# Performance work log

Measured on AMD Instinct MI355X. Metric: run time of the kernel, lower is better.

## Reference

```python
import jax, jax.numpy as jnp
import numpy as np

IN_FEATURES = 4096
OUT_FEATURES = 4096
BANDWIDTH = min(IN_FEATURES, OUT_FEATURES) // 8  # 512, as in the torch default


def band_indices(n_out, n_in, bw):
    """Vectorized equivalent of BandMatrix.create_band_indices (COO row/col lists)."""
    i = np.arange(n_out)
    lo = np.maximum(0, i - bw)
    hi = np.minimum(n_in, i + bw + 1)
    counts = hi - lo
    total = int(counts.sum())
    rows = np.repeat(i, counts)
    start = np.cumsum(counts) - counts  # offset of each row's first entry
    cols = np.arange(total) - np.repeat(start, counts) + np.repeat(lo, counts)
    return rows.astype(np.int32), cols.astype(np.int32)


def setup_inputs() -> dict:
    key = jax.random.key(0)
    kx, kw = jax.random.split(key)
    rows_np, cols_np = band_indices(OUT_FEATURES, IN_FEATURES, BANDWIDTH)
    nnz = rows_np.shape[0]  # 3935744
    x = jax.random.normal(kx, (4, 2048, IN_FEATURES), dtype=jnp.float32)
    W_values = jax.random.normal(kw, (nnz,), dtype=jnp.float32)
    bias = jnp.zeros((OUT_FEATURES,), dtype=jnp.float32)
    return {
        "x": x,
        "W_values": W_values,
        "bias": bias,
        "rows": jnp.asarray(rows_np),
        "cols": jnp.asarray(cols_np),
    }


def reference(x, W_values, bias, rows, cols):
    # Densify banded COO weight [out, in] (matches sparse_coo_tensor().to_dense()).
    W = jnp.zeros((OUT_FEATURES, IN_FEATURES), dtype=W_values.dtype).at[rows, cols].set(W_values)
    # x: [B, S, in] @ W.T: [in, out] -> [B, S, out]
    out = jnp.einsum('bsi,oi->bso', x, W) + bias
    return out
```

## Files before the change

kernel.cpp:

```cpp
#include <hip/hip_runtime.h>
#include <stdint.h>

#define IN_F  4096
#define OUT_F 4096
#define BW    512
#define WB2   1280
#define BM    256
#define BN    256

typedef __bf16 bf16x8 __attribute__((ext_vector_type(8)));
typedef float  f32x4  __attribute__((ext_vector_type(4)));

__device__ __forceinline__ int band_start(int o) {
    if (o <= 512)  return o * 513 + ((o * (o - 1)) >> 1);
    if (o <= 3584) return 393472 + (o - 512) * 1025;
    const int d = o - 3584;
    return 3542272 + (((1024 + 4609 - o) * d) >> 1);
}

__device__ __forceinline__ uint16_t f32_to_bf16(float f) {
    uint32_t u = __builtin_bit_cast(uint32_t, f);
    u += 0x7FFFu + ((u >> 16) & 1u);
    return (uint16_t)(u >> 16);
}

__global__ __launch_bounds__(256) void cvt_x(const float* __restrict__ x,
                                             uint16_t* __restrict__ xb, int n4) {
    const int stride = gridDim.x * 256;
    for (int i = blockIdx.x * 256 + threadIdx.x; i < n4; i += stride) {
        const float4 v = reinterpret_cast<const float4*>(x)[i];
        const uint32_t lo = (uint32_t)f32_to_bf16(v.x) | ((uint32_t)f32_to_bf16(v.y) << 16);
        const uint32_t hi = (uint32_t)f32_to_bf16(v.z) | ((uint32_t)f32_to_bf16(v.w) << 16);
        reinterpret_cast<uint2*>(xb)[i] = make_uint2(lo, hi);
    }
}

__global__ __launch_bounds__(256) void cvt_w(const float* __restrict__ wv,
                                             uint16_t* __restrict__ wd) {
    const int o = blockIdx.y;
    const int j = blockIdx.x * 256 + threadIdx.x;
    const int i = (o & ~(BM - 1)) - BW + j;
    uint16_t v = 0;
    if (i >= o - BW && i <= o + BW && i >= 0 && i < IN_F) {
        const int lo = (o > BW) ? (o - BW) : 0;
        v = f32_to_bf16(wv[band_start(o) + (i - lo)]);
    }
    wd[o * WB2 + j] = v;
}

__global__ __launch_bounds__(512, 1) void band_gemm_v10(
    const uint16_t* __restrict__ xb,
    const uint16_t* __restrict__ wd,
    const float* __restrict__ bias,
    float* __restrict__ out)
{
    __shared__ __align__(128) uint8_t lds[9 * 16384];

    const int id  = blockIdx.x;
    const int bx  = 2 * (id & 7) + ((id >> 3) & 1);
    const int byg = id >> 4;
    const int bcol = bx * BN;
    const int brow0 = byg * BM;

    const int wlo    = bcol - BW;
    const int kstart = wlo > 0 ? wlo : 0;
    const int kend   = (bcol + BN + BW) < IN_F ? (bcol + BN + BW) : IN_F;
    const int nt     = (kend - kstart) >> 6;
    const int j0     = kstart - wlo;

    const int tid  = threadIdx.x;
    const int w    = tid >> 6;
    const int lane = tid & 63;
    const int ln   = lane & 15;
    const int kc   = lane >> 4;
    const int wm   = w >> 2;
    const int wn   = w & 3;

    const int srow = tid >> 3;
    const int csrc = (tid & 7) ^ (srow & 7);
    const uint16_t* aSrc0 = xb + (size_t)(brow0 + srow) * IN_F + kstart + csrc * 8;
    const uint16_t* aSrc1 = aSrc0 + (size_t)16 * BM * IN_F;
    const uint16_t* bSrc  = wd + (size_t)(bcol + srow) * WB2 + j0 + csrc * 8;

#define GLOAD(srcp, dst_off)                                                             \
    __builtin_amdgcn_global_load_lds(                                                    \
        (const __attribute__((address_space(1))) uint32_t*)(srcp),                       \
        (__attribute__((address_space(3))) uint32_t*)(lds + (dst_off) + (w << 10)),      \
        16, 0, 0)

#define STG_UNIT(AS, w_, j_, slot_) {                                                    \
        if (((j_) & 1) == 0) {                                                           \
            const uint16_t* p_ = (AS) + (size_t)(((j_) >> 1) * 128) * IN_F + (w_) * 64;  \
            GLOAD(p_, (slot_) << 14);                                                    \
            GLOAD(p_ + (size_t)64 * IN_F, ((slot_) << 14) + 8192);                       \
        } else {                                                                         \
            const uint16_t* p_ = bSrc + (size_t)(((j_) >> 1) * 128) * WB2 + (w_) * 64;   \
            GLOAD(p_, (slot_) << 14);                                                    \
            GLOAD(p_ + (size_t)64 * WB2, ((slot_) << 14) + 8192);                        \
        } }

    const int cswz = (kc ^ (ln & 7)) << 4;

#define LD_A(BASE, MQ) {                                                                 \
    _Pragma("unroll")                                                                    \
    for (int s_ = 0; s_ < 4; ++s_) {                                                     \
        const int off_ = (BASE) + (((MQ) * 64 + s_ * 16 + ln) << 7) + cswz;              \
        am[s_][0] = *(const bf16x8*)(lds + off_);                                        \
        am[s_][1] = *(const bf16x8*)(lds + (off_ ^ 64));                                 \
    } }
#define LD_B(DST, BASE, NQ) {                                                            \
    _Pragma("unroll")                                                                    \
    for (int s_ = 0; s_ < 2; ++s_) {                                                     \
        const int off_ = (BASE) + (((wn & 1) * 64 + (NQ) * 32 + s_ * 16 + ln) << 7) + cswz; \
        DST[s_][0] = *(const bf16x8*)(lds + off_);                                       \
        DST[s_][1] = *(const bf16x8*)(lds + (off_ ^ 64));                                \
    } }
#define MFMAPH(MROW, NCOL, BB) {                                                         \
    _Pragma("unroll")                                                                    \
    for (int a_ = 0; a_ < 4; ++a_) {                                                     \
        _Pragma("unroll")                                                                \
        for (int n_ = 0; n_ < 2; ++n_) {                                                 \
            acc[(MROW) + a_][(NCOL) + n_] = __builtin_amdgcn_mfma_f32_16x16x32_bf16(     \
                am[a_][0], BB[n_][0], acc[(MROW) + a_][(NCOL) + n_], 0, 0, 0);           \
            acc[(MROW) + a_][(NCOL) + n_] = __builtin_amdgcn_mfma_f32_16x16x32_bf16(     \
                am[a_][1], BB[n_][1], acc[(MROW) + a_][(NCOL) + n_], 0, 0, 0);           \
        } } }

#define PRO(AS) {                                                                        \
    STG_UNIT(AS, 0, 0, 0); STG_UNIT(AS, 0, 1, 1); STG_UNIT(AS, 0, 2, 2);                 \
    STG_UNIT(AS, 0, 3, 3); STG_UNIT(AS, 1, 0, 4); }

#define KLOOP(AS) {                                                                      \
    int s4v = 0;                                                                         \
    for (int v = 0; v < nt; ++v) {                                                       \
        int sA = s4v + (wm << 1);            if (sA >= 9) sA -= 9;                       \
        int sB = s4v + 1 + ((wn >> 1) << 1); if (sB >= 9) sB -= 9;                       \
        const int aBase = sA << 14, bBase = sB << 14;                                    \
        int st0 = s4v + 5; if (st0 >= 9) st0 -= 9;                                       \
        int st1 = st0 + 1; if (st1 >= 9) st1 -= 9;                                       \
        int st2 = st1 + 1; if (st2 >= 9) st2 -= 9;                                       \
        int st3 = st2 + 1; if (st3 >= 9) st3 -= 9;                                       \
        const bool stg_q012 = (v + 1 < nt);                                              \
        const bool stg_q3   = (v + 2 < nt);                                              \
        LD_A(aBase, 0);                                                                  \
        LD_B(bn0, bBase, 0);                                                             \
        if (stg_q012) STG_UNIT(AS, v + 1, 1, st0);                                       \
        MFMAPH(0, 0, bn0);                                                               \
        LD_B(bn1, bBase, 1);                                                             \
        if (stg_q012) STG_UNIT(AS, v + 1, 2, st1);                                       \
        MFMAPH(0, 2, bn1);                                                               \
        LD_A(aBase, 1);                                                                  \
        if (stg_q012) STG_UNIT(AS, v + 1, 3, st2);                                       \
        MFMAPH(4, 2, bn1);                                                               \
        if (stg_q3) STG_UNIT(AS, v + 2, 0, st3);                                         \
        MFMAPH(4, 0, bn0);                                                               \
        if (v + 1 < nt) {                                                                \
            if (v + 2 < nt) { asm volatile("s_waitcnt vmcnt(2)" ::: "memory"); }         \
            else            { asm volatile("s_waitcnt vmcnt(0)" ::: "memory"); }         \
            __builtin_amdgcn_s_barrier();                                                \
        }                                                                                \
        s4v += 4; if (s4v >= 9) s4v -= 9;                                                \
    } }

#define EPI(BROWX) {                                                                     \
    _Pragma("unroll")                                                                    \
    for (int a_ = 0; a_ < 8; ++a_) {                                                     \
        _Pragma("unroll")                                                                \
        for (int q_ = 0; q_ < 4; ++q_) {                                                 \
            const int row_ = (BROWX) + wm * 128 + a_ * 16 + (kc << 2) + q_;              \
            float* po_ = out + (size_t)row_ * OUT_F + ocol;                              \
            _Pragma("unroll")                                                            \
            for (int n_ = 0; n_ < 4; ++n_)                                               \
                po_[n_ * 16] = acc[a_][n_][q_] + bsv[n_];                                 \
        } } }

    const int ocol = bcol + wn * 64 + ln;
    float bsv[4];
    #pragma unroll
    for (int n = 0; n < 4; ++n) bsv[n] = bias[ocol + n * 16];

    f32x4 acc[8][4] = {};
    bf16x8 am[4][2], bn0[2][2], bn1[2][2];

    PRO(aSrc0);
    asm volatile("s_waitcnt vmcnt(2)" ::: "memory");
    __builtin_amdgcn_s_barrier();
    KLOOP(aSrc0);
    __builtin_amdgcn_s_barrier();

    PRO(aSrc1);
    asm volatile("s_waitcnt vmcnt(2)" ::: "memory");
    __builtin_amdgcn_s_barrier();
    EPI(brow0);
    #pragma unroll
    for (int a = 0; a < 8; ++a)
        #pragma unroll
        for (int n = 0; n < 4; ++n) acc[a][n] = (f32x4){0.f, 0.f, 0.f, 0.f};
    KLOOP(aSrc1);
    EPI(brow0 + 16 * BM);

#undef STG_UNIT
#undef GLOAD
#undef PRO
#undef KLOOP
#undef EPI
}

__global__ __launch_bounds__(256) void band_gemm_f32(
    const float* __restrict__ x, const float* __restrict__ wv,
    const float* __restrict__ bias, float* __restrict__ out, int M)
{
    __shared__ float Xs[128][33];
    __shared__ float Ws[32][130];
    const int tid = threadIdx.x;
    const int tx = tid & 15, ty = tid >> 4;
    const int bcol = blockIdx.x * 128, brow = blockIdx.y * 128;
    const int klo = (bcol >= BW) ? (bcol - BW) : 0;
    const int khi = min(IN_F, bcol + 128 + BW);
    float acc[8][8];
    #pragma unroll
    for (int a = 0; a < 8; ++a)
        #pragma unroll
        for (int b = 0; b < 8; ++b) acc[a][b] = 0.f;
    const int xc4 = (tid & 7) * 4, xr0 = tid >> 3;
    const int wc = tid & 31, wr0 = tid >> 5;
    for (int k0 = klo; k0 < khi; k0 += 32) {
        #pragma unroll
        for (int p = 0; p < 4; ++p) {
            const int rr = xr0 + 32 * p;
            const float4 v = *reinterpret_cast<const float4*>(&x[(size_t)(brow + rr) * IN_F + (k0 + xc4)]);
            Xs[rr][xc4 + 0] = v.x; Xs[rr][xc4 + 1] = v.y; Xs[rr][xc4 + 2] = v.z; Xs[rr][xc4 + 3] = v.w;
        }
        const int i = k0 + wc;
        #pragma unroll
        for (int p = 0; p < 16; ++p) {
            const int rr = wr0 + 8 * p;
            const int o = bcol + rr;
            const int lo = (o >= BW) ? (o - BW) : 0;
            float v = 0.f;
            if (i >= o - BW && i <= o + BW) v = wv[band_start(o) + (i - lo)];
            Ws[wc][rr] = v;
        }
        __syncthreads();
        #pragma unroll
        for (int k = 0; k < 32; ++k) {
            float amv[8];
            #pragma unroll
            for (int a = 0; a < 8; ++a) amv[a] = Xs[ty * 8 + a][k];
            float bo[8];
            #pragma unroll
            for (int b = 0; b < 4; ++b) { bo[b] = Ws[k][tx * 4 + b]; bo[4 + b] = Ws[k][tx * 4 + 64 + b]; }
            #pragma unroll
            for (int a = 0; a < 8; ++a)
                #pragma unroll
                for (int b = 0; b < 8; ++b) acc[a][b] = fmaf(amv[a], bo[b], acc[a][b]);
        }
        __syncthreads();
    }
    #pragma unroll
    for (int a = 0; a < 8; ++a) {
        const size_t row = (size_t)(brow + ty * 8 + a);
        #pragma unroll
        for (int b = 0; b < 4; ++b) {
            out[row * OUT_F + bcol + tx * 4 + b]      = acc[a][b]     + bias[bcol + tx * 4 + b];
            out[row * OUT_F + bcol + tx * 4 + 64 + b] = acc[a][4 + b] + bias[bcol + tx * 4 + 64 + b];
        }
    }
}

extern "C" void kernel_launch(void* const* d_in, const int* in_sizes, int n_in,
                              void* d_out, int out_size, void* d_ws, size_t ws_size,
                              hipStream_t stream) {
    const float* x    = (const float*)d_in[0];
    const float* wv   = (const float*)d_in[1];
    const float* bias = (const float*)d_in[2];
    float* out        = (float*)d_out;

    const int M = in_sizes[0] / IN_F;
    const size_t xb_bytes = (size_t)M * IN_F * 2;
    const size_t wd_bytes = (size_t)OUT_F * WB2 * 2;

    if (ws_size >= xb_bytes + wd_bytes && M == 8192) {
        uint16_t* xb  = (uint16_t*)d_ws;
        uint16_t* wdp = (uint16_t*)((uint8_t*)d_ws + xb_bytes);
        cvt_x<<<2048, 256, 0, stream>>>(x, xb, M * IN_F / 4);
        cvt_w<<<dim3(WB2 / 256, OUT_F), 256, 0, stream>>>(wv, wdp);
        band_gemm_v10<<<256, 512, 0, stream>>>(xb, wdp, bias, out);
    } else {
        dim3 grid(OUT_F / 128, M / 128);
        band_gemm_f32<<<grid, 256, 0, stream>>>(x, wv, bias, out, M);
    }
}
```

Measured before the change: 139.3 us.

## Fuse fp32-to-bf16 conversion of x into GEMM A-tile staging with double buffering

Drops the separate cvt_x pass. The GEMM now reads fp32 x directly into registers, converts it with v_cvt_pk_bf16_f32 and writes bf16 into LDS, while B tiles still use direct global-to-LDS loads. The 9-slot rotating pipeline becomes a simple two-stage double buffer that waits for all loads and syncs at every K step. This removes a full write and read of the bf16 copy of x, but doubles the global bytes read for A inside the GEMM, adds register pressure, and gives a shallower prefetch pipeline with full waits.

New measurement: 155.4 us. 1.12x slower.

```diff
diff --git a/kernel.cpp b/kernel.cpp
--- a/kernel.cpp
+++ b/kernel.cpp
@@ -22,17 +22,6 @@
     uint32_t u = __builtin_bit_cast(uint32_t, f);
     u += 0x7FFFu + ((u >> 16) & 1u);
     return (uint16_t)(u >> 16);
-}
-
-__global__ __launch_bounds__(256) void cvt_x(const float* __restrict__ x,
-                                             uint16_t* __restrict__ xb, int n4) {
-    const int stride = gridDim.x * 256;
-    for (int i = blockIdx.x * 256 + threadIdx.x; i < n4; i += stride) {
-        const float4 v = reinterpret_cast<const float4*>(x)[i];
-        const uint32_t lo = (uint32_t)f32_to_bf16(v.x) | ((uint32_t)f32_to_bf16(v.y) << 16);
-        const uint32_t hi = (uint32_t)f32_to_bf16(v.z) | ((uint32_t)f32_to_bf16(v.w) << 16);
-        reinterpret_cast<uint2*>(xb)[i] = make_uint2(lo, hi);
-    }
 }
 
 __global__ __launch_bounds__(256) void cvt_w(const float* __restrict__ wv,
@@ -48,13 +37,13 @@
     wd[o * WB2 + j] = v;
 }
 
-__global__ __launch_bounds__(512, 1) void band_gemm_v10(
-    const uint16_t* __restrict__ xb,
+__global__ __launch_bounds__(512, 1) void band_gemm_v11(
+    const float* __restrict__ xf,
     const uint16_t* __restrict__ wd,
     const float* __restrict__ bias,
     float* __restrict__ out)
 {
-    __shared__ __align__(128) uint8_t lds[9 * 16384];
+    __shared__ __align__(128) uint8_t lds[131072];
 
     const int id  = blockIdx.x;
     const int bx  = 2 * (id & 7) + ((id >> 3) & 1);
@@ -78,9 +67,9 @@
 
     const int srow = tid >> 3;
     const int csrc = (tid & 7) ^ (srow & 7);
-    const uint16_t* aSrc0 = xb + (size_t)(brow0 + srow) * IN_F + kstart + csrc * 8;
-    const uint16_t* aSrc1 = aSrc0 + (size_t)16 * BM * IN_F;
-    const uint16_t* bSrc  = wd + (size_t)(bcol + srow) * WB2 + j0 + csrc * 8;
+    const float*    aF0  = xf + (size_t)(brow0 + srow) * IN_F + kstart + csrc * 8;
+    const float*    aF1  = aF0 + (size_t)16 * BM * IN_F;
+    const uint16_t* bSrc = wd + (size_t)(bcol + srow) * WB2 + j0 + csrc * 8;
 
 #define GLOAD(srcp, dst_off)                                                             \
     __builtin_amdgcn_global_load_lds(                                                    \
@@ -88,32 +77,49 @@
         (__attribute__((address_space(3))) uint32_t*)(lds + (dst_off) + (w << 10)),      \
         16, 0, 0)
 
-#define STG_UNIT(AS, w_, j_, slot_) {                                                    \
-        if (((j_) & 1) == 0) {                                                           \
-            const uint16_t* p_ = (AS) + (size_t)(((j_) >> 1) * 128) * IN_F + (w_) * 64;  \
-            GLOAD(p_, (slot_) << 14);                                                    \
-            GLOAD(p_ + (size_t)64 * IN_F, ((slot_) << 14) + 8192);                       \
-        } else {                                                                         \
-            const uint16_t* p_ = bSrc + (size_t)(((j_) >> 1) * 128) * WB2 + (w_) * 64;   \
-            GLOAD(p_, (slot_) << 14);                                                    \
-            GLOAD(p_ + (size_t)64 * WB2, ((slot_) << 14) + 8192);                        \
-        } }
+#define STG_B(tv_, h_, bb_) { const uint16_t* p_ = bSrc + (size_t)((h_) * 128) * WB2 + (tv_) * 64; \
+        GLOAD(p_, (bb_) + 32768 + (h_) * 16384);                                         \
+        GLOAD(p_ + (size_t)64 * WB2, (bb_) + 32768 + (h_) * 16384 + 8192); }
+
+    float4 rA[4][2];
+#define A_ISSUE(AF, tv_) {                                                               \
+    _Pragma("unroll")                                                                    \
+    for (int r_ = 0; r_ < 4; ++r_) {                                                     \
+        const float* p_ = (AF) + (size_t)(r_ * 64) * IN_F + (tv_) * 64;                  \
+        rA[r_][0] = *(const float4*)p_;                                                  \
+        rA[r_][1] = *(const float4*)(p_ + 4);                                            \
+    } }
+#define A_WRITE(pair_, bb_) {                                                            \
+    _Pragma("unroll")                                                                    \
+    for (int r_ = 0; r_ < 2; ++r_) {                                                     \
+        const int rr_ = (pair_) * 2 + r_;                                                \
+        uint32_t d0_, d1_, d2_, d3_;                                                     \
+        asm("v_cvt_pk_bf16_f32 %0, %1, %2" : "=v"(d0_) : "v"(rA[rr_][0].x), "v"(rA[rr_][0].y)); \
+        asm("v_cvt_pk_bf16_f32 %0, %1, %2" : "=v"(d1_) : "v"(rA[rr_][0].z), "v"(rA[rr_][0].w)); \
+        asm("v_cvt_pk_bf16_f32 %0, %1, %2" : "=v"(d2_) : "v"(rA[rr_][1].x), "v"(rA[rr_][1].y)); \
+        asm("v_cvt_pk_bf16_f32 %0, %1, %2" : "=v"(d3_) : "v"(rA[rr_][1].z), "v"(rA[rr_][1].w)); \
+        *(uint4*)(lds + (bb_) + rr_ * 8192 + tid * 16) = make_uint4(d0_, d1_, d2_, d3_); \
+    } }
 
     const int cswz = (kc ^ (ln & 7)) << 4;
-
-#define LD_A(BASE, MQ) {                                                                 \
+    int aOff[8], bOff[4];
+    #pragma unroll
+    for (int a = 0; a < 8; ++a) aOff[a] = ((wm * 128 + a * 16 + ln) << 7) + cswz;
+    #pragma unroll
+    for (int n = 0; n < 4; ++n) bOff[n] = 32768 + ((wn * 64 + n * 16 + ln) << 7) + cswz;
+
+    bf16x8 am[4][2], bn0[2][2], bn1[2][2];
+#define LD_A(BB, MQ) {                                                                   \
     _Pragma("unroll")                                                                    \
     for (int s_ = 0; s_ < 4; ++s_) {                                                     \
-        const int off_ = (BASE) + (((MQ) * 64 + s_ * 16 + ln) << 7) + cswz;              \
-        am[s_][0] = *(const bf16x8*)(lds + off_);                                        \
-        am[s_][1] = *(const bf16x8*)(lds + (off_ ^ 64));                                 \
-    } }
-#define LD_B(DST, BASE, NQ) {                                                            \
+        am[s_][0] = *(const bf16x8*)(lds + (BB) + aOff[(MQ) * 4 + s_]);                  \
+        am[s_][1] = *(const bf16x8*)(lds + (BB) + (aOff[(MQ) * 4 + s_] ^ 64));           \
+    } }
+#define LD_B(DST, BB, NQ) {                                                              \
     _Pragma("unroll")                                                                    \
     for (int s_ = 0; s_ < 2; ++s_) {                                                     \
-        const int off_ = (BASE) + (((wn & 1) * 64 + (NQ) * 32 + s_ * 16 + ln) << 7) + cswz; \
-        DST[s_][0] = *(const bf16x8*)(lds + off_);                                       \
-        DST[s_][1] = *(const bf16x8*)(lds + (off_ ^ 64));                                \
+        DST[s_][0] = *(const bf16x8*)(lds + (BB) + bOff[(NQ) * 2 + s_]);                 \
+        DST[s_][1] = *(const bf16x8*)(lds + (BB) + (bOff[(NQ) * 2 + s_] ^ 64));          \
     } }
 #define MFMAPH(MROW, NCOL, BB) {                                                         \
     _Pragma("unroll")                                                                    \
@@ -126,40 +132,38 @@
                 am[a_][1], BB[n_][1], acc[(MROW) + a_][(NCOL) + n_], 0, 0, 0);           \
         } } }
 
-#define PRO(AS) {                                                                        \
-    STG_UNIT(AS, 0, 0, 0); STG_UNIT(AS, 0, 1, 1); STG_UNIT(AS, 0, 2, 2);                 \
-    STG_UNIT(AS, 0, 3, 3); STG_UNIT(AS, 1, 0, 4); }
-
-#define KLOOP(AS) {                                                                      \
-    int s4v = 0;                                                                         \
+#define BOUNDARY  asm volatile("s_waitcnt vmcnt(0)" ::: "memory");                       \
+                  asm volatile("s_waitcnt lgkmcnt(0)" ::: "memory");                     \
+                  __builtin_amdgcn_s_barrier();                                          \
+                  asm volatile("" ::: "memory")
+
+#define PRO(AF) {                                                                        \
+    A_ISSUE(AF, 0);                                                                      \
+    STG_B(0, 0, 0); STG_B(0, 1, 0);                                                      \
+    A_WRITE(0, 0); A_WRITE(1, 0);                                                        \
+    BOUNDARY; }
+
+#define KLOOP(AF) {                                                                      \
     for (int v = 0; v < nt; ++v) {                                                       \
-        int sA = s4v + (wm << 1);            if (sA >= 9) sA -= 9;                       \
-        int sB = s4v + 1 + ((wn >> 1) << 1); if (sB >= 9) sB -= 9;                       \
-        const int aBase = sA << 14, bBase = sB << 14;                                    \
-        int st0 = s4v + 5; if (st0 >= 9) st0 -= 9;                                       \
-        int st1 = st0 + 1; if (st1 >= 9) st1 -= 9;                                       \
-        int st2 = st1 + 1; if (st2 >= 9) st2 -= 9;                                       \
-        int st3 = st2 + 1; if (st3 >= 9) st3 -= 9;                                       \
-        const bool stg_q012 = (v + 1 < nt);                                              \
-        const bool stg_q3   = (v + 2 < nt);                                              \
-        LD_A(aBase, 0);                                                                  \
-        LD_B(bn0, bBase, 0);                                                             \
-        if (stg_q012) STG_UNIT(AS, v + 1, 1, st0);                                       \
+        const int cur = (v & 1) << 16;                                                   \
+        const int nxt = cur ^ 65536;                                                     \
+        const bool st = (v + 1 < nt);                                                    \
+                                                                                 \
+        LD_A(cur, 0); LD_B(bn0, cur, 0);                                                 \
+        if (st) A_ISSUE(AF, v + 1);                                                      \
         MFMAPH(0, 0, bn0);                                                               \
-        LD_B(bn1, bBase, 1);                                                             \
-        if (stg_q012) STG_UNIT(AS, v + 1, 2, st1);                                       \
+                                                                                 \
+        LD_B(bn1, cur, 1);                                                               \
+        if (st) STG_B(v + 1, 0, nxt);                                                    \
         MFMAPH(0, 2, bn1);                                                               \
-        LD_A(aBase, 1);                                                                  \
-        if (stg_q012) STG_UNIT(AS, v + 1, 3, st2);                                       \
+                                                                                 \
+        LD_A(cur, 1);                                                                    \
+        if (st) A_WRITE(0, nxt);                                                         \
         MFMAPH(4, 2, bn1);                                                               \
-        if (stg_q3) STG_UNIT(AS, v + 2, 0, st3);                                         \
+                                                                                 \
+        if (st) { STG_B(v + 1, 1, nxt); A_WRITE(1, nxt); }                               \
         MFMAPH(4, 0, bn0);                                                               \
-        if (v + 1 < nt) {                                                                \
-            if (v + 2 < nt) { asm volatile("s_waitcnt vmcnt(2)" ::: "memory"); }         \
-            else            { asm volatile("s_waitcnt vmcnt(0)" ::: "memory"); }         \
-            __builtin_amdgcn_s_barrier();                                                \
-        }                                                                                \
-        s4v += 4; if (s4v >= 9) s4v -= 9;                                                \
+        BOUNDARY;                                                                        \
     } }
 
 #define EPI(BROWX) {                                                                     \
@@ -180,27 +184,26 @@
     for (int n = 0; n < 4; ++n) bsv[n] = bias[ocol + n * 16];
 
     f32x4 acc[8][4] = {};
-    bf16x8 am[4][2], bn0[2][2], bn1[2][2];
-
-    PRO(aSrc0);
-    asm volatile("s_waitcnt vmcnt(2)" ::: "memory");
-    __builtin_amdgcn_s_barrier();
-    KLOOP(aSrc0);
-    __builtin_amdgcn_s_barrier();
-
-    PRO(aSrc1);
-    asm volatile("s_waitcnt vmcnt(2)" ::: "memory");
-    __builtin_amdgcn_s_barrier();
+
+    PRO(aF0);
+    KLOOP(aF0);
+    PRO(aF1);
     EPI(brow0);
     #pragma unroll
     for (int a = 0; a < 8; ++a)
         #pragma unroll
         for (int n = 0; n < 4; ++n) acc[a][n] = (f32x4){0.f, 0.f, 0.f, 0.f};
-    KLOOP(aSrc1);
+    KLOOP(aF1);
     EPI(brow0 + 16 * BM);
 
-#undef STG_UNIT
 #undef GLOAD
+#undef STG_B
+#undef A_ISSUE
+#undef A_WRITE
+#undef LD_A
+#undef LD_B
+#undef MFMAPH
+#undef BOUNDARY
 #undef PRO
 #undef KLOOP
 #undef EPI
@@ -277,15 +280,12 @@
     float* out        = (float*)d_out;
 
     const int M = in_sizes[0] / IN_F;
-    const size_t xb_bytes = (size_t)M * IN_F * 2;
     const size_t wd_bytes = (size_t)OUT_F * WB2 * 2;
 
-    if (ws_size >= xb_bytes + wd_bytes && M == 8192) {
-        uint16_t* xb  = (uint16_t*)d_ws;
-        uint16_t* wdp = (uint16_t*)((uint8_t*)d_ws + xb_bytes);
-        cvt_x<<<2048, 256, 0, stream>>>(x, xb, M * IN_F / 4);
+    if (ws_size >= wd_bytes && M == 8192) {
+        uint16_t* wdp = (uint16_t*)d_ws;
         cvt_w<<<dim3(WB2 / 256, OUT_F), 256, 0, stream>>>(wv, wdp);
-        band_gemm_v10<<<256, 512, 0, stream>>>(xb, wdp, bias, out);
+        band_gemm_v11<<<256, 512, 0, stream>>>(x, wdp, bias, out);
     } else {
         dim3 grid(OUT_F / 128, M / 128);
         band_gemm_f32<<<grid, 256, 0, stream>>>(x, wv, bias, out, M);
```
